# Kernel tuning notes

Hardware: AMD Instinct MI355X
Metric: run time of the kernel (lower is better)

## Reference

```python
import jax, jax.numpy as jnp
import numpy as np

B, T, NF, T2V, GH, NH, GRUH = 128, 256, 17, 16, 32, 4, 128


def _t2v(t, w0, b0, W, Bp):
    # t: [...] -> [..., T2V] = [linear term, sin periodic terms]
    lin = t[..., None] * w0 + b0
    per = jnp.sin(t[..., None] * W + Bp)
    return jnp.concatenate([lin, per], axis=-1)


def _gat(h, adj, W, a_src, a_dst, residual):
    # h: [N, F, Din], W: [Din, H, O], a_*: [H, O]; batched multi-head GAT over N graphs
    p = jnp.einsum('nfd,dho->nfho', h, W)
    es = jnp.einsum('nfho,ho->nhf', p, a_src)
    ed = jnp.einsum('nfho,ho->nhf', p, a_dst)
    e = jax.nn.leaky_relu(es[:, :, :, None] + ed[:, :, None, :], 0.2)  # [N,H,F,F]
    e = jnp.where(adj[None, None] > 0, e, jnp.float32(-1e9))
    a = jax.nn.softmax(e, axis=-1)
    out = jnp.einsum('nhij,njho->niho', a, p).reshape(h.shape[0], h.shape[1], -1)
    if residual:
        out = out + h
    return jax.nn.elu(out)


def _gru_dir(x, wih, whh, bih, bhh, reverse):
    # PyTorch GRU gate order [r, z, n]; x: [B,T,D] -> (outputs [B,T,H], h_final [B,H])
    gx = jnp.einsum('btd,gd->btg', x, wih) + bih
    if reverse:
        gx = gx[:, ::-1]
    H = whh.shape[1]

    def step(h, gxt):
        gh = h @ whh.T + bhh
        r = jax.nn.sigmoid(gxt[:, :H] + gh[:, :H])
        z = jax.nn.sigmoid(gxt[:, H:2 * H] + gh[:, H:2 * H])
        n = jnp.tanh(gxt[:, 2 * H:] + r * gh[:, 2 * H:])
        h2 = (1.0 - z) * n + z * h
        return h2, h2

    h0 = jnp.zeros((x.shape[0], H), x.dtype)
    hT, ys = jax.lax.scan(step, h0, jnp.swapaxes(gx, 0, 1))
    ys = jnp.swapaxes(ys, 0, 1)
    if reverse:
        ys = ys[:, ::-1]
    return ys, hT


def setup_inputs() -> dict:
    key = jax.random.key(0)
    ks = iter(jax.random.split(key, 64))

    def nrm(shape, fan):
        return jax.random.normal(next(ks), shape, jnp.float32) / np.float32(np.sqrt(fan))

    X = jax.random.normal(next(ks), (B, T, NF), jnp.float32)
    mask = (jax.random.uniform(next(ks), (B, T, NF)) > 0.3).astype(jnp.float32)
    delta = jax.random.uniform(next(ks), (B, T, NF), jnp.float32) * 10.0
    times = jnp.broadcast_to(jnp.arange(T, dtype=jnp.float32)[None], (B, T)) + jax.random.uniform(next(ks), (B, T), jnp.float32)
    adj = jnp.ones((NF, NF), jnp.float32) - jnp.eye(NF, dtype=jnp.float32)

    D0 = 2 + 2 * T2V  # node_in_dim = 34
    GO = GH * NH      # gat_out_dim = 128
    inp = dict(X=X, mask=mask, delta=delta, times=times, adj=adj,
               aw0=nrm((1,), 1), ab0=nrm((1,), 1), aW=nrm((T2V - 1,), 1), aB=nrm((T2V - 1,), 1),
               dw0=nrm((1,), 1), db0=nrm((1,), 1), dW=nrm((T2V - 1,), 1), dB=nrm((T2V - 1,), 1),
               gW0=nrm((D0, NH, GH), D0), gas0=nrm((NH, GH), GH), gad0=nrm((NH, GH), GH),
               gW1=nrm((GO, NH, GH), GO), gas1=nrm((NH, GH), GH), gad1=nrm((NH, GH), GH))
    for name, ind in [('g0f', GO), ('g0b', GO), ('g1f', 2 * GRUH), ('g1b', 2 * GRUH)]:
        inp[name + '_wih'] = nrm((3 * GRUH, ind), ind)
        inp[name + '_whh'] = nrm((3 * GRUH, GRUH), GRUH)
        inp[name + '_bih'] = jnp.zeros((3 * GRUH,), jnp.float32)
        inp[name + '_bhh'] = jnp.zeros((3 * GRUH,), jnp.float32)
    pd = 2 * GRUH
    inp.update(mh_w1=nrm((64, pd), pd), mh_b1=jnp.zeros((64,), jnp.float32),
               mh_w2=nrm((1, 64), 64), mh_b2=jnp.zeros((1,), jnp.float32),
               ch_w1=nrm((64, pd), pd), ch_b1=jnp.zeros((64,), jnp.float32),
               ch_w2=nrm((1, 64), 64), ch_b2=jnp.zeros((1,), jnp.float32))
    return inp


def reference(X, mask, delta, times, adj, aw0, ab0, aW, aB, dw0, db0, dW, dB,
              gW0, gas0, gad0, gW1, gas1, gad1,
              g0f_wih, g0f_whh, g0f_bih, g0f_bhh, g0b_wih, g0b_whh, g0b_bih, g0b_bhh,
              g1f_wih, g1f_whh, g1f_bih, g1f_bhh, g1b_wih, g1b_whh, g1b_bih, g1b_bhh,
              mh_w1, mh_b1, mh_w2, mh_b2, ch_w1, ch_b1, ch_w2, ch_b2):
    Bx, Tx, F = X.shape
    # node features: [x, mask, time2vec(t), time2vec(delta)] -> [B,T,F,34]
    t_emb = _t2v(times, aw0, ab0, aW, aB)
    t_emb = jnp.broadcast_to(t_emb[:, :, None, :], (Bx, Tx, F, T2V))
    d_emb = _t2v(delta, dw0, db0, dW, dB)
    nf = jnp.concatenate([X[..., None], mask[..., None], t_emb, d_emb], axis=-1)
    # batched GAT over all B*T graphs at once (replaces the Python bt-loop)
    h = nf.reshape(Bx * Tx, F, nf.shape[-1])
    h = _gat(h, adj, gW0, gas0, gad0, False)
    h = _gat(h, adj, gW1, gas1, gad1, True)
    z = h.mean(axis=1).reshape(Bx, Tx, NH * GH)
    # bidirectional 2-layer GRU
    yf, _ = _gru_dir(z, g0f_wih, g0f_whh, g0f_bih, g0f_bhh, False)
    yb, _ = _gru_dir(z, g0b_wih, g0b_whh, g0b_bih, g0b_bhh, True)
    y = jnp.concatenate([yf, yb], axis=-1)
    yf1, hf1 = _gru_dir(y, g1f_wih, g1f_whh, g1f_bih, g1f_bhh, False)
    yb1, hb1 = _gru_dir(y, g1b_wih, g1b_whh, g1b_bih, g1b_bhh, True)
    gru_out = jnp.concatenate([yf1, yb1], axis=-1)
    patient_emb = jnp.concatenate([hf1, hb1], axis=-1)
    m = jax.nn.relu(patient_emb @ mh_w1.T + mh_b1) @ mh_w2.T + mh_b2
    risk = jax.nn.relu(patient_emb @ ch_w1.T + ch_b1) @ ch_w2.T + ch_b2
    return (m, jax.nn.sigmoid(m), risk, patient_emb, gru_out)
```

## Files before the change

kernel.cpp:

```cpp
#include <hip/hip_runtime.h>
#include <hip/hip_bf16.h>
#include <math.h>

#define NFE 17
#define T2V 16
#define D0C 34
#define BB 128
#define TT 256
#define HH 128
#define PSTR 132
#define ASTR 136

typedef __hip_bfloat16 bf16;
__device__ __forceinline__ float b2f(bf16 x) { return __bfloat162float(x); }

typedef __attribute__((ext_vector_type(8))) __bf16 bfrag;
typedef __attribute__((ext_vector_type(4))) float  ffrag;
typedef __attribute__((ext_vector_type(4))) __bf16 bf4;

__device__ __forceinline__ float elu_fast(float v)  { return v > 0.f ? v : __expf(v) - 1.f; }
__device__ __forceinline__ float sigm_fast(float x) { return __fdividef(1.f, 1.f + __expf(-x)); }
__device__ __forceinline__ float tanh_fast(float x) {
  return __fdividef(2.f, 1.f + __expf(-2.f*x)) - 1.f;
}

__device__ __bf16 g_W0h[8192],  g_W0l[8192];
__device__ __bf16 g_W1h[16384], g_W1l[16384];

__global__ __launch_bounds__(256) void prep_w(const float* __restrict__ W0,
                                              const float* __restrict__ W1) {
  const int tid = blockIdx.x*256 + threadIdx.x;
  if (tid < 16384) {
    const int j = tid & 7, lane = (tid >> 3) & 63, ks = (tid >> 9) & 3, nt = tid >> 11;
    const int n = nt*16 + (lane & 15), k = ks*32 + (lane >> 4)*8 + j;
    const float v = W1[k*128 + n];
    const __bf16 hi = (__bf16)v;
    g_W1h[tid] = hi;
    g_W1l[tid] = (__bf16)(v - (float)hi);
  }
  if (tid < 8192) {
    const int j = tid & 7, lane = (tid >> 3) & 63, ks = (tid >> 9) & 1, nt = tid >> 10;
    const int n = nt*16 + (lane & 15), k = ks*32 + (lane >> 4)*8 + j;
    const float v = (k < D0C) ? W0[k*128 + n] : 0.f;
    const __bf16 hi = (__bf16)v;
    g_W0h[tid] = hi;
    g_W0l[tid] = (__bf16)(v - (float)hi);
  }
}

template<int KSTEPS>
__device__ __forceinline__ void gat_proj_mfma(const __bf16* s_ah, const __bf16* s_al,
                                              const __bf16* __restrict__ Wth,
                                              const __bf16* __restrict__ Wtl,
                                              float* s_p, __bf16* s_pth, __bf16* s_ptl,
                                              int tid)
{
  const int lane = tid & 63, wv = tid >> 6;
  const int mn = lane & 15, q = lane >> 4;
  ffrag acc[2][2] = {};
  #pragma unroll
  for (int ks = 0; ks < KSTEPS; ++ks) {
    const bfrag ah0 = *(const bfrag*)&s_ah[(     mn)*ASTR + ks*32 + q*8];
    const bfrag al0 = *(const bfrag*)&s_al[(     mn)*ASTR + ks*32 + q*8];
    const bfrag ah1 = *(const bfrag*)&s_ah[(16 + mn)*ASTR + ks*32 + q*8];
    const bfrag al1 = *(const bfrag*)&s_al[(16 + mn)*ASTR + ks*32 + q*8];
    #pragma unroll
    for (int nt = 0; nt < 2; ++nt) {
      const int fi = (((wv*2 + nt)*KSTEPS + ks)*64 + lane)*8;
      const bfrag bh = *(const bfrag*)&Wth[fi];
      const bfrag bl = *(const bfrag*)&Wtl[fi];
      acc[0][nt] = __builtin_amdgcn_mfma_f32_16x16x32_bf16(al0, bh, acc[0][nt], 0,0,0);
      acc[0][nt] = __builtin_amdgcn_mfma_f32_16x16x32_bf16(ah0, bl, acc[0][nt], 0,0,0);
      acc[0][nt] = __builtin_amdgcn_mfma_f32_16x16x32_bf16(ah0, bh, acc[0][nt], 0,0,0);
      acc[1][nt] = __builtin_amdgcn_mfma_f32_16x16x32_bf16(al1, bh, acc[1][nt], 0,0,0);
      acc[1][nt] = __builtin_amdgcn_mfma_f32_16x16x32_bf16(ah1, bl, acc[1][nt], 0,0,0);
      acc[1][nt] = __builtin_amdgcn_mfma_f32_16x16x32_bf16(ah1, bh, acc[1][nt], 0,0,0);
    }
  }
  const int n0 = wv*32;
  #pragma unroll
  for (int nt = 0; nt < 2; ++nt) {
    const int col = n0 + nt*16 + mn;
    #pragma unroll
    for (int i = 0; i < 4; ++i) {
      const float v = acc[0][nt][i];
      s_p[(q*4 + i)*PSTR + col] = v;
      const __bf16 hi = (__bf16)v;
      s_pth[col*32 + q*4 + i] = hi;
      s_ptl[col*32 + q*4 + i] = (__bf16)(v - (float)hi);
    }
    if (q == 0) {
      const float v = acc[1][nt][0];
      s_p[16*PSTR + col] = v;
      const __bf16 hi = (__bf16)v;
      s_pth[col*32 + 16] = hi;
      s_ptl[col*32 + 16] = (__bf16)(v - (float)hi);
    }
  }
}

__device__ __forceinline__ void gat_scores(const float* s_p,
                                           const float* __restrict__ asrc,
                                           const float* __restrict__ adst,
                                           float* s_es, float* s_ed, int tid) {
  if (tid < 2*4*NFE) {
    const int which = tid >= 4*NFE;
    const int r = which ? tid - 4*NFE : tid;
    const int h = r / NFE, f = r - h*NFE;
    const float* av = which ? adst : asrc;
    float acc = 0.f;
    #pragma unroll
    for (int o = 0; o < 32; o += 4) {
      const float4 p4 = *(const float4*)&s_p[f*PSTR + h*32 + o];
      const float4 a4 = *(const float4*)&av[h*32 + o];
      acc = fmaf(p4.x, a4.x, acc);
      acc = fmaf(p4.y, a4.y, acc);
      acc = fmaf(p4.z, a4.z, acc);
      acc = fmaf(p4.w, a4.w, acc);
    }
    (which ? s_ed : s_es)[h*NFE + f] = acc;
  }
}

__device__ __forceinline__ void gat_softmax(const float* s_es, const float* s_ed,
                                            const float* s_adj,
                                            __bf16* s_Eh, __bf16* s_El, int tid) {
  if (tid < 4*NFE) {
    const int h = tid / NFE, i = tid - h*NFE;
    float row[NFE]; float mx = -1e30f;
    #pragma unroll
    for (int j = 0; j < NFE; ++j) {
      float v = -1.0e9f;
      if (s_adj[i*NFE + j] > 0.f) {
        float e = s_es[h*NFE + i] + s_ed[h*NFE + j];
        v = (e > 0.f) ? e : 0.2f*e;
      }
      row[j] = v; mx = fmaxf(mx, v);
    }
    float sum = 0.f;
    #pragma unroll
    for (int j = 0; j < NFE; ++j) { row[j] = __expf(row[j] - mx); sum += row[j]; }
    const float inv = __fdividef(1.f, sum);
    #pragma unroll
    for (int j = 0; j < NFE; ++j) {
      const float v = row[j]*inv;
      const __bf16 hi = (__bf16)v;
      s_Eh[h*544 + i*32 + j] = hi;
      s_El[h*544 + i*32 + j] = (__bf16)(v - (float)hi);
    }
  }
}

__device__ __forceinline__ void gat_out0_mfma(const __bf16* s_Eh, const __bf16* s_El,
                                              const __bf16* s_pth, const __bf16* s_ptl,
                                              __bf16* s_ah, __bf16* s_al, int tid) {
  const int lane = tid & 63, wv = tid >> 6;
  const int mn = lane & 15, q = lane >> 4;
  ffrag acc[2][2] = {};
  const bfrag eh0 = *(const bfrag*)&s_Eh[wv*544 + mn*32 + q*8];
  const bfrag el0 = *(const bfrag*)&s_El[wv*544 + mn*32 + q*8];
  const bfrag eh1 = *(const bfrag*)&s_Eh[wv*544 + (16+mn)*32 + q*8];
  const bfrag el1 = *(const bfrag*)&s_El[wv*544 + (16+mn)*32 + q*8];
  #pragma unroll
  for (int nt = 0; nt < 2; ++nt) {
    const int nrow = wv*32 + nt*16 + mn;
    const bfrag ph = *(const bfrag*)&s_pth[nrow*32 + q*8];
    const bfrag pl = *(const bfrag*)&s_ptl[nrow*32 + q*8];
    acc[0][nt] = __builtin_amdgcn_mfma_f32_16x16x32_bf16(el0, ph, acc[0][nt], 0,0,0);
    acc[0][nt] = __builtin_amdgcn_mfma_f32_16x16x32_bf16(eh0, pl, acc[0][nt], 0,0,0);
    acc[0][nt] = __builtin_amdgcn_mfma_f32_16x16x32_bf16(eh0, ph, acc[0][nt], 0,0,0);
    acc[1][nt] = __builtin_amdgcn_mfma_f32_16x16x32_bf16(el1, ph, acc[1][nt], 0,0,0);
    acc[1][nt] = __builtin_amdgcn_mfma_f32_16x16x32_bf16(eh1, pl, acc[1][nt], 0,0,0);
    acc[1][nt] = __builtin_amdgcn_mfma_f32_16x16x32_bf16(eh1, ph, acc[1][nt], 0,0,0);
  }
  #pragma unroll
  for (int nt = 0; nt < 2; ++nt) {
    const int c = wv*32 + nt*16 + mn;
    #pragma unroll
    for (int i = 0; i < 4; ++i) {
      const float v = elu_fast(acc[0][nt][i]);
      const __bf16 hi = (__bf16)v;
      s_ah[(q*4+i)*ASTR + c] = hi;
      s_al[(q*4+i)*ASTR + c] = (__bf16)(v - (float)hi);
    }
    if (q == 0) {
      const float v = elu_fast(acc[1][nt][0]);
      const __bf16 hi = (__bf16)v;
      s_ah[16*ASTR + c] = hi;
      s_al[16*ASTR + c] = (__bf16)(v - (float)hi);
    }
  }
}

__device__ __forceinline__ void gat_out1_mfma(const __bf16* s_Eh, const __bf16* s_El,
                                              const __bf16* s_pth, const __bf16* s_ptl,
                                              const __bf16* s_ah, const __bf16* s_al,
                                              float* __restrict__ zrow, int tid) {
  const int lane = tid & 63, wv = tid >> 6;
  const int mn = lane & 15, q = lane >> 4;
  ffrag acc[2][2] = {};
  const bfrag eh0 = *(const bfrag*)&s_Eh[wv*544 + mn*32 + q*8];
  const bfrag el0 = *(const bfrag*)&s_El[wv*544 + mn*32 + q*8];
  const bfrag eh1 = *(const bfrag*)&s_Eh[wv*544 + (16+mn)*32 + q*8];
  const bfrag el1 = *(const bfrag*)&s_El[wv*544 + (16+mn)*32 + q*8];
  #pragma unroll
  for (int nt = 0; nt < 2; ++nt) {
    const int nrow = wv*32 + nt*16 + mn;
    const bfrag ph = *(const bfrag*)&s_pth[nrow*32 + q*8];
    const bfrag pl = *(const bfrag*)&s_ptl[nrow*32 + q*8];
    acc[0][nt] = __builtin_amdgcn_mfma_f32_16x16x32_bf16(el0, ph, acc[0][nt], 0,0,0);
    acc[0][nt] = __builtin_amdgcn_mfma_f32_16x16x32_bf16(eh0, pl, acc[0][nt], 0,0,0);
    acc[0][nt] = __builtin_amdgcn_mfma_f32_16x16x32_bf16(eh0, ph, acc[0][nt], 0,0,0);
    acc[1][nt] = __builtin_amdgcn_mfma_f32_16x16x32_bf16(el1, ph, acc[1][nt], 0,0,0);
    acc[1][nt] = __builtin_amdgcn_mfma_f32_16x16x32_bf16(eh1, pl, acc[1][nt], 0,0,0);
    acc[1][nt] = __builtin_amdgcn_mfma_f32_16x16x32_bf16(eh1, ph, acc[1][nt], 0,0,0);
  }
  #pragma unroll
  for (int nt = 0; nt < 2; ++nt) {
    const int c = wv*32 + nt*16 + mn;
    float sum = 0.f;
    #pragma unroll
    for (int i = 0; i < 4; ++i) {
      const int r = q*4 + i;
      const float res = (float)s_ah[r*ASTR + c] + (float)s_al[r*ASTR + c];
      sum += elu_fast(acc[0][nt][i] + res);
    }
    sum += __shfl_xor(sum, 16);
    sum += __shfl_xor(sum, 32);
    if (q == 0) {
      const float res = (float)s_ah[16*ASTR + c] + (float)s_al[16*ASTR + c];
      sum += elu_fast(acc[1][nt][0] + res);
      zrow[c] = sum * (1.0f/17.0f);
    }
  }
}

__global__ __launch_bounds__(256) void gat_fused(
    const float* __restrict__ X,  const float* __restrict__ Mk,
    const float* __restrict__ Dl, const float* __restrict__ Tm,
    const float* __restrict__ Adj,
    const float* __restrict__ aw0, const float* __restrict__ ab0,
    const float* __restrict__ aW,  const float* __restrict__ aB,
    const float* __restrict__ dw0, const float* __restrict__ db0,
    const float* __restrict__ dW,  const float* __restrict__ dB,
    const float* __restrict__ as0, const float* __restrict__ ad0,
    const float* __restrict__ as1, const float* __restrict__ ad1,
    float* __restrict__ zslot)
{
  __shared__ __align__(16) unsigned char smem[45088];
  __bf16* s_ah  = (__bf16*)(smem);
  __bf16* s_al  = (__bf16*)(smem + 4624);
  float*  s_p   = (float*)(smem + 9248);
  __bf16* s_pth = (__bf16*)(smem + 18224);
  __bf16* s_ptl = (__bf16*)(smem + 26416);
  __bf16* s_Eh  = (__bf16*)(smem + 34608);
  __bf16* s_El  = (__bf16*)(smem + 38960);
  float*  s_es  = (float*)(smem + 43312);
  float*  s_ed  = (float*)(smem + 43584);
  float*  s_t   = (float*)(smem + 43856);
  float*  s_adj = (float*)(smem + 43920);
  const int n = blockIdx.x;
  const int tid = threadIdx.x;

  {
    const float4 z4 = {0.f, 0.f, 0.f, 0.f};
    float4* zp = (float4*)(smem + 18224);
    for (int i = tid; i < 1568; i += 256) zp[i] = z4;
  }
  const float tv = Tm[n];
  if (tid < T2V) {
    s_t[tid] = (tid == 0) ? fmaf(tv, aw0[0], ab0[0])
                          : __sinf(fmaf(tv, aW[tid-1], aB[tid-1]));
  }
  for (int idx = tid; idx < NFE*NFE; idx += 256) s_adj[idx] = Adj[idx];
  __syncthreads();
  for (int idx = tid; idx < NFE*64; idx += 256) {
    const int f = idx >> 6, c = idx & 63;
    float v = 0.f;
    if (c == 0)            v = X [(size_t)n*NFE + f];
    else if (c == 1)       v = Mk[(size_t)n*NFE + f];
    else if (c < 2 + T2V)  v = s_t[c-2];
    else if (c < D0C) {
      const float dd = Dl[(size_t)n*NFE + f];
      const int j = c - (2 + T2V);
      v = (j == 0) ? fmaf(dd, dw0[0], db0[0])
                   : __sinf(fmaf(dd, dW[j-1], dB[j-1]));
    }
    const __bf16 hi = (__bf16)v;
    s_ah[f*ASTR + c] = hi;
    s_al[f*ASTR + c] = (__bf16)(v - (float)hi);
  }
  __syncthreads();
  gat_proj_mfma<2>(s_ah, s_al, g_W0h, g_W0l, s_p, s_pth, s_ptl, tid); __syncthreads();
  gat_scores(s_p, as0, ad0, s_es, s_ed, tid);                         __syncthreads();
  gat_softmax(s_es, s_ed, s_adj, s_Eh, s_El, tid);                    __syncthreads();
  gat_out0_mfma(s_Eh, s_El, s_pth, s_ptl, s_ah, s_al, tid);           __syncthreads();
  gat_proj_mfma<4>(s_ah, s_al, g_W1h, g_W1l, s_p, s_pth, s_ptl, tid); __syncthreads();
  gat_scores(s_p, as1, ad1, s_es, s_ed, tid);                         __syncthreads();
  gat_softmax(s_es, s_ed, s_adj, s_Eh, s_El, tid);                    __syncthreads();
  gat_out1_mfma(s_Eh, s_El, s_pth, s_ptl, s_ah, s_al,
                zslot + (size_t)n*256 + 128, tid);
}

__global__ __launch_bounds__(256) void gemm_xw_mfma(
    const float* __restrict__ A, int lda, const float* __restrict__ W,
    const float* __restrict__ bias, bf16* __restrict__ C, int K)
{
  __shared__ __bf16 Ah[64][40];
  __shared__ __bf16 Al[64][40];
  __shared__ __bf16 Wh[64][40];
  __shared__ __bf16 Wl[64][40];
  const int tid = threadIdx.x;
  const int bm0 = blockIdx.x * 64;
  const int bn0 = blockIdx.y * 64;
  const int lane = tid & 63, wv = tid >> 6;
  const int mn = lane & 15, q = lane >> 4;
  const int sr = tid >> 2, sk = (tid & 3) * 8;
  ffrag acc[4] = {};
  for (int kk = 0; kk < K; kk += 32) {
    {
      float av[8];
      *(float4*)&av[0] = *(const float4*)&A[(size_t)(bm0 + sr)*lda + kk + sk];
      *(float4*)&av[4] = *(const float4*)&A[(size_t)(bm0 + sr)*lda + kk + sk + 4];
      __bf16 th[8], tl[8];
      #pragma unroll
      for (int i = 0; i < 8; ++i) {
        const __bf16 hi = (__bf16)av[i];
        th[i] = hi;
        tl[i] = (__bf16)(av[i] - (float)hi);
      }
      *(bfrag*)&Ah[sr][sk] = *(bfrag*)th;
      *(bfrag*)&Al[sr][sk] = *(bfrag*)tl;
      float wv8[8];
      *(float4*)&wv8[0] = *(const float4*)&W[(size_t)(bn0 + sr)*K + kk + sk];
      *(float4*)&wv8[4] = *(const float4*)&W[(size_t)(bn0 + sr)*K + kk + sk + 4];
      __bf16 wh8[8], wl8[8];
      #pragma unroll
      for (int i = 0; i < 8; ++i) {
        const __bf16 hi = (__bf16)wv8[i];
        wh8[i] = hi;
        wl8[i] = (__bf16)(wv8[i] - (float)hi);
      }
      *(bfrag*)&Wh[sr][sk] = *(bfrag*)wh8;
      *(bfrag*)&Wl[sr][sk] = *(bfrag*)wl8;
    }
    __syncthreads();
    const bfrag afh = *(const bfrag*)&Ah[16*wv + mn][q*8];
    const bfrag afl = *(const bfrag*)&Al[16*wv + mn][q*8];
    #pragma unroll
    for (int t = 0; t < 4; ++t) {
      const bfrag bwh = *(const bfrag*)&Wh[16*t + mn][q*8];
      const bfrag bwl = *(const bfrag*)&Wl[16*t + mn][q*8];
      acc[t] = __builtin_amdgcn_mfma_f32_16x16x32_bf16(afl, bwh, acc[t], 0, 0, 0);
      acc[t] = __builtin_amdgcn_mfma_f32_16x16x32_bf16(afh, bwl, acc[t], 0, 0, 0);
      acc[t] = __builtin_amdgcn_mfma_f32_16x16x32_bf16(afh, bwh, acc[t], 0, 0, 0);
    }
    __syncthreads();
  }
  #pragma unroll
  for (int t = 0; t < 4; ++t) {
    const int col = bn0 + 16*t + mn;
    const float bv = bias[col];
    #pragma unroll
    for (int i = 0; i < 4; ++i) {
      const int row = bm0 + 16*wv + q*4 + i;
      C[(size_t)row*384 + col] = __float2bfloat16(acc[t][i] + bv);
    }
  }
}

__global__ __launch_bounds__(384, 1) void gru_rec(
    const bf16* __restrict__ gxf,
    const bf16* __restrict__ gxb,
    const float* __restrict__ whh_f, const float* __restrict__ whh_b,
    const float* __restrict__ bhh_f, const float* __restrict__ bhh_b,
    float* __restrict__ ys,
    float* __restrict__ hfin)
{
  const int blk = blockIdx.x;
  const int dir = blk >> 7;
  const int b   = blk & 127;
  const int g   = threadIdx.x;
  const float* whh = dir ? whh_b : whh_f;
  const float* bhh = dir ? bhh_b : bhh_f;
  const bf16* gx   = (dir ? gxb : gxf) + (size_t)b*TT*384;
  __shared__ __align__(16) float s_h[HH];
  __shared__ float s_gh[3*HH];
  __shared__ float s_gx[3*HH];
  float4 w[HH/4];
  #pragma unroll
  for (int d4 = 0; d4 < HH/4; ++d4)
    w[d4] = *(const float4*)&whh[(size_t)g*HH + 4*d4];
  const float bh = bhh[g];
  float hreg = 0.f;
  if (g < HH) s_h[g] = 0.f;
  __syncthreads();
  for (int s = 0; s < TT; ++s) {
    const int t = dir ? (TT-1-s) : s;
    const float gxv = b2f(gx[(size_t)t*384 + g]);
    float acc = bh;
    const float4* h4 = (const float4*)s_h;
    #pragma unroll
    for (int d4 = 0; d4 < HH/4; ++d4) {
      const float4 hv = h4[d4];
      acc = fmaf(hv.x, w[d4].x, acc);
      acc = fmaf(hv.y, w[d4].y, acc);
      acc = fmaf(hv.z, w[d4].z, acc);
      acc = fmaf(hv.w, w[d4].w, acc);
    }
    s_gh[g] = acc;
    s_gx[g] = gxv;
    __syncthreads();
    if (g < HH) {
      const float r  = sigm_fast(s_gx[g]    + s_gh[g]);
      const float zg = sigm_fast(s_gx[HH+g] + s_gh[HH+g]);
      const float nn = tanh_fast(s_gx[2*HH+g] + r*s_gh[2*HH+g]);
      hreg = (1.f - zg)*nn + zg*hreg;
      s_h[g] = hreg;
      ys[((size_t)b*TT + t)*256 + dir*HH + g] = hreg;
    }
    __syncthreads();
  }
  if (g < HH && hfin) hfin[(size_t)b*256 + dir*HH + g] = hreg;
}

__global__ __launch_bounds__(64) void heads_k(
    const float* __restrict__ pemb,
    const float* __restrict__ mw1, const float* __restrict__ mb1,
    const float* __restrict__ mw2, const float* __restrict__ mb2,
    const float* __restrict__ cw1, const float* __restrict__ cb1,
    const float* __restrict__ cw2, const float* __restrict__ cb2,
    float* __restrict__ out)
{
  const int b = blockIdx.x, tid = threadIdx.x;
  __shared__ float sh[64];
  const float* pe = pemb + (size_t)b*256;
  float acc = mb1[tid];
  for (int d = 0; d < 256; ++d) acc = fmaf(pe[d], mw1[(size_t)tid*256 + d], acc);
  sh[tid] = fmaxf(acc, 0.f) * mw2[tid];
  __syncthreads();
  if (tid == 0) {
    float s = mb2[0];
    for (int i = 0; i < 64; ++i) s += sh[i];
    out[b]       = s;
    out[128 + b] = 1.f/(1.f + expf(-s));
  }
  __syncthreads();
  acc = cb1[tid];
  for (int d = 0; d < 256; ++d) acc = fmaf(pe[d], cw1[(size_t)tid*256 + d], acc);
  sh[tid] = fmaxf(acc, 0.f) * cw2[tid];
  __syncthreads();
  if (tid == 0) {
    float s = cb2[0];
    for (int i = 0; i < 64; ++i) s += sh[i];
    out[256 + b] = s;
  }
}

extern "C" void kernel_launch(void* const* d_in, const int* in_sizes, int n_in,
                              void* d_out, int out_size, void* d_ws, size_t ws_size,
                              hipStream_t stream) {
  const float* X    = (const float*)d_in[0];
  const float* Mk   = (const float*)d_in[1];
  const float* Dl   = (const float*)d_in[2];
  const float* Tm   = (const float*)d_in[3];
  const float* Adj  = (const float*)d_in[4];
  const float* aw0  = (const float*)d_in[5];
  const float* ab0  = (const float*)d_in[6];
  const float* aWt  = (const float*)d_in[7];
  const float* aBt  = (const float*)d_in[8];
  const float* dw0  = (const float*)d_in[9];
  const float* db0  = (const float*)d_in[10];
  const float* dWt  = (const float*)d_in[11];
  const float* dBt  = (const float*)d_in[12];
  const float* gW0  = (const float*)d_in[13];
  const float* gas0 = (const float*)d_in[14];
  const float* gad0 = (const float*)d_in[15];
  const float* gW1  = (const float*)d_in[16];
  const float* gas1 = (const float*)d_in[17];
  const float* gad1 = (const float*)d_in[18];
  const float* g0f_wih = (const float*)d_in[19];
  const float* g0f_whh = (const float*)d_in[20];
  const float* g0f_bih = (const float*)d_in[21];
  const float* g0f_bhh = (const float*)d_in[22];
  const float* g0b_wih = (const float*)d_in[23];
  const float* g0b_whh = (const float*)d_in[24];
  const float* g0b_bih = (const float*)d_in[25];
  const float* g0b_bhh = (const float*)d_in[26];
  const float* g1f_wih = (const float*)d_in[27];
  const float* g1f_whh = (const float*)d_in[28];
  const float* g1f_bih = (const float*)d_in[29];
  const float* g1f_bhh = (const float*)d_in[30];
  const float* g1b_wih = (const float*)d_in[31];
  const float* g1b_whh = (const float*)d_in[32];
  const float* g1b_bih = (const float*)d_in[33];
  const float* g1b_bhh = (const float*)d_in[34];
  const float* mh_w1 = (const float*)d_in[35];
  const float* mh_b1 = (const float*)d_in[36];
  const float* mh_w2 = (const float*)d_in[37];
  const float* mh_b2 = (const float*)d_in[38];
  const float* ch_w1 = (const float*)d_in[39];
  const float* ch_b1 = (const float*)d_in[40];
  const float* ch_w2 = (const float*)d_in[41];
  const float* ch_b2 = (const float*)d_in[42];

  bf16* gxA = (bf16*)d_ws;
  bf16* gxB = gxA + 12582912;

  float* out  = (float*)d_out;
  float* pemb = out + 384;
  float* slot = out + 384 + 32768;

  prep_w<<<64, 256, 0, stream>>>(gW0, gW1);

  gat_fused<<<dim3(BB*TT), dim3(256), 0, stream>>>(
      X, Mk, Dl, Tm, Adj, aw0, ab0, aWt, aBt, dw0, db0, dWt, dBt,
      gas0, gad0, gas1, gad1, slot);

  dim3 ggrid(32768/64, 384/64);
  gemm_xw_mfma<<<ggrid, 256, 0, stream>>>(slot + 128, 256, g0f_wih, g0f_bih, gxA, 128);
  gemm_xw_mfma<<<ggrid, 256, 0, stream>>>(slot + 128, 256, g0b_wih, g0b_bih, gxB, 128);
  gru_rec<<<256, 384, 0, stream>>>(gxA, gxB, g0f_whh, g0b_whh, g0f_bhh, g0b_bhh,
                                   slot, nullptr);
  gemm_xw_mfma<<<ggrid, 256, 0, stream>>>(slot, 256, g1f_wih, g1f_bih, gxA, 256);
  gemm_xw_mfma<<<ggrid, 256, 0, stream>>>(slot, 256, g1b_wih, g1b_bih, gxB, 256);
  gru_rec<<<256, 384, 0, stream>>>(gxA, gxB, g1f_whh, g1b_whh, g1f_bhh, g1b_bhh,
                                   slot, pemb);

  heads_k<<<128, 64, 0, stream>>>(pemb, mh_w1, mh_b1, mh_w2, mh_b2,
                                  ch_w1, ch_b1, ch_w2, ch_b2, out);
}
```

Measured before the change: 1.264 ms.

## Fuse GAT softmax into attention MFMA and pad transposed projection layout

The separate softmax stage, which wrote bf16 hi/lo attention matrices to shared memory, is removed. Each wave now computes the attention softmax rows it needs in registers and packs them straight into MFMA A-fragments. This drops two barriers and the attention shared buffers. The transposed projection buffers use a padded stride of 40 with vectorized 4-element stores, which is meant to reduce bank conflicts and store count. In exchange, every lane redundantly computes softmax rows (17 exps twice per lane) instead of one thread per row, which adds ALU work.

```diff
diff --git a/kernel.cpp b/kernel.cpp
--- a/kernel.cpp
+++ b/kernel.cpp
@@ -10,6 +10,7 @@
 #define HH 128
 #define PSTR 132
 #define ASTR 136
+#define KSTR 40
 
 typedef __hip_bfloat16 bf16;
 __device__ __forceinline__ float b2f(bf16 x) { return __bfloat162float(x); }
@@ -81,20 +82,23 @@
   #pragma unroll
   for (int nt = 0; nt < 2; ++nt) {
     const int col = n0 + nt*16 + mn;
+    __bf16 hbuf[4], lbuf[4];
     #pragma unroll
     for (int i = 0; i < 4; ++i) {
       const float v = acc[0][nt][i];
       s_p[(q*4 + i)*PSTR + col] = v;
       const __bf16 hi = (__bf16)v;
-      s_pth[col*32 + q*4 + i] = hi;
-      s_ptl[col*32 + q*4 + i] = (__bf16)(v - (float)hi);
-    }
+      hbuf[i] = hi;
+      lbuf[i] = (__bf16)(v - (float)hi);
+    }
+    *(bf4*)&s_pth[col*KSTR + q*4] = *(bf4*)hbuf;
+    *(bf4*)&s_ptl[col*KSTR + q*4] = *(bf4*)lbuf;
     if (q == 0) {
       const float v = acc[1][nt][0];
       s_p[16*PSTR + col] = v;
       const __bf16 hi = (__bf16)v;
-      s_pth[col*32 + 16] = hi;
-      s_ptl[col*32 + 16] = (__bf16)(v - (float)hi);
+      s_pth[col*KSTR + 16] = hi;
+      s_ptl[col*KSTR + 16] = (__bf16)(v - (float)hi);
     }
   }
 }
@@ -122,50 +126,59 @@
   }
 }
 
-__device__ __forceinline__ void gat_softmax(const float* s_es, const float* s_ed,
-                                            const float* s_adj,
-                                            __bf16* s_Eh, __bf16* s_El, int tid) {
-  if (tid < 4*NFE) {
-    const int h = tid / NFE, i = tid - h*NFE;
-    float row[NFE]; float mx = -1e30f;
-    #pragma unroll
-    for (int j = 0; j < NFE; ++j) {
-      float v = -1.0e9f;
-      if (s_adj[i*NFE + j] > 0.f) {
-        float e = s_es[h*NFE + i] + s_ed[h*NFE + j];
-        v = (e > 0.f) ? e : 0.2f*e;
-      }
-      row[j] = v; mx = fmaxf(mx, v);
-    }
-    float sum = 0.f;
-    #pragma unroll
-    for (int j = 0; j < NFE; ++j) { row[j] = __expf(row[j] - mx); sum += row[j]; }
-    const float inv = __fdividef(1.f, sum);
-    #pragma unroll
-    for (int j = 0; j < NFE; ++j) {
-      const float v = row[j]*inv;
-      const __bf16 hi = (__bf16)v;
-      s_Eh[h*544 + i*32 + j] = hi;
-      s_El[h*544 + i*32 + j] = (__bf16)(v - (float)hi);
-    }
-  }
-}
-
-__device__ __forceinline__ void gat_out0_mfma(const __bf16* s_Eh, const __bf16* s_El,
-                                              const __bf16* s_pth, const __bf16* s_ptl,
-                                              __bf16* s_ah, __bf16* s_al, int tid) {
-  const int lane = tid & 63, wv = tid >> 6;
-  const int mn = lane & 15, q = lane >> 4;
-  ffrag acc[2][2] = {};
-  const bfrag eh0 = *(const bfrag*)&s_Eh[wv*544 + mn*32 + q*8];
-  const bfrag el0 = *(const bfrag*)&s_El[wv*544 + mn*32 + q*8];
-  const bfrag eh1 = *(const bfrag*)&s_Eh[wv*544 + (16+mn)*32 + q*8];
-  const bfrag el1 = *(const bfrag*)&s_El[wv*544 + (16+mn)*32 + q*8];
+__device__ __forceinline__ void softmax_row(const float* s_es, const float* s_ed,
+                                            const float* s_adj, int h, int i,
+                                            float* row, float& inv) {
+  float mx = -1e30f;
+  const float esv = s_es[h*NFE + i];
+  #pragma unroll
+  for (int j = 0; j < NFE; ++j) {
+    float v = -1.0e9f;
+    if (s_adj[i*NFE + j] > 0.f) {
+      const float e = esv + s_ed[h*NFE + j];
+      v = (e > 0.f) ? e : 0.2f*e;
+    }
+    row[j] = v; mx = fmaxf(mx, v);
+  }
+  float sum = 0.f;
+  #pragma unroll
+  for (int j = 0; j < NFE; ++j) { row[j] = __expf(row[j] - mx); sum += row[j]; }
+  inv = __fdividef(1.f, sum);
+}
+
+__device__ __forceinline__ void pack_slice(const float* row, float inv, int q,
+                                           int keep, bfrag* ph, bfrag* pl) {
+  __bf16 hbuf[8], lbuf[8];
+  #pragma unroll
+  for (int jj = 0; jj < 8; ++jj) {
+    float v = 0.f;
+    if (q == 0)      v = row[jj] * inv;
+    else if (q == 1) v = row[8 + jj] * inv;
+    else if (q == 2) { if (jj == 0) v = row[16] * inv; }
+    if (!keep) v = 0.f;
+    const __bf16 hi = (__bf16)v;
+    hbuf[jj] = hi;
+    lbuf[jj] = (__bf16)(v - (float)hi);
+  }
+  *ph = *(bfrag*)hbuf;
+  *pl = *(bfrag*)lbuf;
+}
+
+__device__ __forceinline__ void gat_out_core(const float* s_es, const float* s_ed,
+                                             const float* s_adj,
+                                             const __bf16* s_pth, const __bf16* s_ptl,
+                                             int wv, int mn, int q, ffrag acc[2][2]) {
+  float row[NFE]; float inv;
+  bfrag eh0, el0, eh1, el1;
+  softmax_row(s_es, s_ed, s_adj, wv, mn, row, inv);
+  pack_slice(row, inv, q, 1, &eh0, &el0);
+  softmax_row(s_es, s_ed, s_adj, wv, 16, row, inv);
+  pack_slice(row, inv, q, mn == 0 ? 1 : 0, &eh1, &el1);
   #pragma unroll
   for (int nt = 0; nt < 2; ++nt) {
     const int nrow = wv*32 + nt*16 + mn;
-    const bfrag ph = *(const bfrag*)&s_pth[nrow*32 + q*8];
-    const bfrag pl = *(const bfrag*)&s_ptl[nrow*32 + q*8];
+    const bfrag ph = *(const bfrag*)&s_pth[nrow*KSTR + q*8];
+    const bfrag pl = *(const bfrag*)&s_ptl[nrow*KSTR + q*8];
     acc[0][nt] = __builtin_amdgcn_mfma_f32_16x16x32_bf16(el0, ph, acc[0][nt], 0,0,0);
     acc[0][nt] = __builtin_amdgcn_mfma_f32_16x16x32_bf16(eh0, pl, acc[0][nt], 0,0,0);
     acc[0][nt] = __builtin_amdgcn_mfma_f32_16x16x32_bf16(eh0, ph, acc[0][nt], 0,0,0);
@@ -173,6 +186,16 @@
     acc[1][nt] = __builtin_amdgcn_mfma_f32_16x16x32_bf16(eh1, pl, acc[1][nt], 0,0,0);
     acc[1][nt] = __builtin_amdgcn_mfma_f32_16x16x32_bf16(eh1, ph, acc[1][nt], 0,0,0);
   }
+}
+
+__device__ __forceinline__ void gat_out0(const float* s_es, const float* s_ed,
+                                         const float* s_adj,
+                                         const __bf16* s_pth, const __bf16* s_ptl,
+                                         __bf16* s_ah, __bf16* s_al, int tid) {
+  const int lane = tid & 63, wv = tid >> 6;
+  const int mn = lane & 15, q = lane >> 4;
+  ffrag acc[2][2] = {};
+  gat_out_core(s_es, s_ed, s_adj, s_pth, s_ptl, wv, mn, q, acc);
   #pragma unroll
   for (int nt = 0; nt < 2; ++nt) {
     const int c = wv*32 + nt*16 + mn;
@@ -192,29 +215,15 @@
   }
 }
 
-__device__ __forceinline__ void gat_out1_mfma(const __bf16* s_Eh, const __bf16* s_El,
-                                              const __bf16* s_pth, const __bf16* s_ptl,
-                                              const __bf16* s_ah, const __bf16* s_al,
-                                              float* __restrict__ zrow, int tid) {
+__device__ __forceinline__ void gat_out1(const float* s_es, const float* s_ed,
+                                         const float* s_adj,
+                                         const __bf16* s_pth, const __bf16* s_ptl,
+                                         const __bf16* s_ah, const __bf16* s_al,
+                                         float* __restrict__ zrow, int tid) {
   const int lane = tid & 63, wv = tid >> 6;
   const int mn = lane & 15, q = lane >> 4;
   ffrag acc[2][2] = {};
-  const bfrag eh0 = *(const bfrag*)&s_Eh[wv*544 + mn*32 + q*8];
-  const bfrag el0 = *(const bfrag*)&s_El[wv*544 + mn*32 + q*8];
-  const bfrag eh1 = *(const bfrag*)&s_Eh[wv*544 + (16+mn)*32 + q*8];
-  const bfrag el1 = *(const bfrag*)&s_El[wv*544 + (16+mn)*32 + q*8];
-  #pragma unroll
-  for (int nt = 0; nt < 2; ++nt) {
-    const int nrow = wv*32 + nt*16 + mn;
-    const bfrag ph = *(const bfrag*)&s_pth[nrow*32 + q*8];
-    const bfrag pl = *(const bfrag*)&s_ptl[nrow*32 + q*8];
-    acc[0][nt] = __builtin_amdgcn_mfma_f32_16x16x32_bf16(el0, ph, acc[0][nt], 0,0,0);
-    acc[0][nt] = __builtin_amdgcn_mfma_f32_16x16x32_bf16(eh0, pl, acc[0][nt], 0,0,0);
-    acc[0][nt] = __builtin_amdgcn_mfma_f32_16x16x32_bf16(eh0, ph, acc[0][nt], 0,0,0);
-    acc[1][nt] = __builtin_amdgcn_mfma_f32_16x16x32_bf16(el1, ph, acc[1][nt], 0,0,0);
-    acc[1][nt] = __builtin_amdgcn_mfma_f32_16x16x32_bf16(eh1, pl, acc[1][nt], 0,0,0);
-    acc[1][nt] = __builtin_amdgcn_mfma_f32_16x16x32_bf16(eh1, ph, acc[1][nt], 0,0,0);
-  }
+  gat_out_core(s_es, s_ed, s_adj, s_pth, s_ptl, wv, mn, q, acc);
   #pragma unroll
   for (int nt = 0; nt < 2; ++nt) {
     const int c = wv*32 + nt*16 + mn;
@@ -247,25 +256,23 @@
     const float* __restrict__ as1, const float* __restrict__ ad1,
     float* __restrict__ zslot)
 {
-  __shared__ __align__(16) unsigned char smem[45088];
+  __shared__ __align__(16) unsigned char smem[40480];
   __bf16* s_ah  = (__bf16*)(smem);
   __bf16* s_al  = (__bf16*)(smem + 4624);
   float*  s_p   = (float*)(smem + 9248);
   __bf16* s_pth = (__bf16*)(smem + 18224);
-  __bf16* s_ptl = (__bf16*)(smem + 26416);
-  __bf16* s_Eh  = (__bf16*)(smem + 34608);
-  __bf16* s_El  = (__bf16*)(smem + 38960);
-  float*  s_es  = (float*)(smem + 43312);
-  float*  s_ed  = (float*)(smem + 43584);
-  float*  s_t   = (float*)(smem + 43856);
-  float*  s_adj = (float*)(smem + 43920);
+  __bf16* s_ptl = (__bf16*)(smem + 28464);
+  float*  s_es  = (float*)(smem + 38704);
+  float*  s_ed  = (float*)(smem + 38976);
+  float*  s_t   = (float*)(smem + 39248);
+  float*  s_adj = (float*)(smem + 39312);
   const int n = blockIdx.x;
   const int tid = threadIdx.x;
 
   {
     const float4 z4 = {0.f, 0.f, 0.f, 0.f};
     float4* zp = (float4*)(smem + 18224);
-    for (int i = tid; i < 1568; i += 256) zp[i] = z4;
+    for (int i = tid; i < 1280; i += 256) zp[i] = z4;
   }
   const float tv = Tm[n];
   if (tid < T2V) {
@@ -293,13 +300,11 @@
   __syncthreads();
   gat_proj_mfma<2>(s_ah, s_al, g_W0h, g_W0l, s_p, s_pth, s_ptl, tid); __syncthreads();
   gat_scores(s_p, as0, ad0, s_es, s_ed, tid);                         __syncthreads();
-  gat_softmax(s_es, s_ed, s_adj, s_Eh, s_El, tid);                    __syncthreads();
-  gat_out0_mfma(s_Eh, s_El, s_pth, s_ptl, s_ah, s_al, tid);           __syncthreads();
+  gat_out0(s_es, s_ed, s_adj, s_pth, s_ptl, s_ah, s_al, tid);         __syncthreads();
   gat_proj_mfma<4>(s_ah, s_al, g_W1h, g_W1l, s_p, s_pth, s_ptl, tid); __syncthreads();
   gat_scores(s_p, as1, ad1, s_es, s_ed, tid);                         __syncthreads();
-  gat_softmax(s_es, s_ed, s_adj, s_Eh, s_El, tid);                    __syncthreads();
-  gat_out1_mfma(s_Eh, s_El, s_pth, s_ptl, s_ah, s_al,
-                zslot + (size_t)n*256 + 128, tid);
+  gat_out1(s_es, s_ed, s_adj, s_pth, s_ptl, s_ah, s_al,
+           zslot + (size_t)n*256 + 128, tid);
 }
 
 __global__ __launch_bounds__(256) void gemm_xw_mfma(
```

Result: no change. 1.262 ms (-0.2%).
